# Kernel tuning notes

Hardware: AMD Instinct MI355X
Metric: run time of the kernel (lower is better)

Reference implementation:

```python
import jax, jax.numpy as jnp
import numpy as np

N, E, S, G = 524288, 2097152, 8192, 64
F_IN, HID = 64, 128


def setup_inputs() -> dict:
    key = jax.random.key(0)
    ks = jax.random.split(key, 12)
    x = jax.random.normal(ks[0], (N, F_IN), dtype=jnp.float32)
    edge_index = jax.random.randint(ks[1], (2, E), 0, N, dtype=jnp.int64)
    node_batch = jnp.sort(jax.random.randint(ks[2], (N,), 0, S, dtype=jnp.int64))
    weights = jax.random.uniform(ks[3], (S, 1), dtype=jnp.float32)
    subgraph_batch = jnp.sort(jax.random.randint(ks[4], (S,), 0, G, dtype=jnp.int64))
    s = 1.0 / np.sqrt(F_IN)
    h = 1.0 / np.sqrt(HID)
    W_l = jax.random.uniform(ks[5], (F_IN, HID), jnp.float32, -s, s)
    W_r = jax.random.uniform(ks[6], (F_IN, HID), jnp.float32, -s, s)
    b_conv = jax.random.uniform(ks[7], (HID,), jnp.float32, -s, s)
    W1 = jax.random.uniform(ks[8], (HID, HID), jnp.float32, -h, h)
    b1 = jax.random.uniform(ks[9], (HID,), jnp.float32, -h, h)
    W2 = jax.random.uniform(ks[10], (HID, 1), jnp.float32, -h, h)
    b2 = jax.random.uniform(ks[11], (1,), jnp.float32, -h, h)
    return {"x": x, "edge_index": edge_index, "node_batch": node_batch,
            "weights": weights, "subgraph_batch": subgraph_batch,
            "W_l": W_l, "W_r": W_r, "b_conv": b_conv,
            "W1": W1, "b1": b1, "W2": W2, "b2": b2}


def reference(x, edge_index, node_batch, weights, subgraph_batch,
              W_l, W_r, b_conv, W1, b1, W2, b2):
    src, dst = edge_index[0], edge_index[1]
    # GraphSAGE mean aggregation: gather neighbor feats, scatter-mean to dst
    msg_sum = jax.ops.segment_sum(x[src], dst, num_segments=N)  # [N, F_IN]
    deg = jax.ops.segment_sum(jnp.ones((E,), x.dtype), dst, num_segments=N)
    agg = msg_sum / jnp.maximum(deg, 1.0)[:, None]
    h = jax.nn.relu(agg @ W_l + x @ W_r + b_conv)               # [N, HID]
    # global_add_pool nodes -> subgraph embeddings
    g = jax.ops.segment_sum(h, node_batch, num_segments=S)      # [S, HID]
    # MLP head -> scalar per subgraph
    s = jax.nn.leaky_relu(g @ W1 + b1, negative_slope=0.01) @ W2 + b2  # [S, 1]
    sw = s * weights
    energy = jax.ops.segment_sum(sw, subgraph_batch, num_segments=G)   # [G, 1]
    norm = jax.ops.segment_sum(weights, subgraph_batch, num_segments=G)
    return energy / norm
```

## Files before the change

### kernel.cpp

```cpp
#include <hip/hip_runtime.h>
#include <hip/hip_bf16.h>

#define NN 524288
#define NE 2097152
#define NS 8192
#define NG 64
#define FIN 64
#define HIDDEN 128

#define NB 512
#define BIN_NODES 1024
#define CAP 4608

typedef __attribute__((ext_vector_type(8))) unsigned short ushort8;
typedef __attribute__((ext_vector_type(4))) unsigned short ushort4v;
typedef __attribute__((ext_vector_type(8))) short bf16x8;
typedef __attribute__((ext_vector_type(4))) float floatx4;

__device__ __forceinline__ unsigned short f2b(float f) {
  union { float f; unsigned int u; } c; c.f = f;
  unsigned int u = c.u;
  unsigned int r = (u + 0x7FFFu + ((u >> 16) & 1u)) >> 16;
  return (unsigned short)r;
}
__device__ __forceinline__ float b2f(unsigned short b) {
  union { unsigned int u; float f; } c; c.u = ((unsigned int)b) << 16;
  return c.f;
}

__global__ __launch_bounds__(256) void k_cast(const float* __restrict__ x,
                                              unsigned short* __restrict__ xb) {
  size_t i = ((size_t)blockIdx.x * 256 + threadIdx.x) * 8;
  float4 v0 = *(const float4*)(x + i);
  float4 v1 = *(const float4*)(x + i + 4);
  ushort8 r;
  r[0] = f2b(v0.x); r[1] = f2b(v0.y); r[2] = f2b(v0.z); r[3] = f2b(v0.w);
  r[4] = f2b(v1.x); r[5] = f2b(v1.y); r[6] = f2b(v1.z); r[7] = f2b(v1.w);
  *(ushort8*)(xb + i) = r;
}

__global__ __launch_bounds__(256) void k_prepw(const float* __restrict__ Wl,
                                               const float* __restrict__ Wr,
                                               unsigned short* __restrict__ Wt) {
  int i = blockIdx.x * 256 + threadIdx.x;
  int n = i >> 7, k = i & 127;
  float v = (k < FIN) ? Wl[k * HIDDEN + n] : Wr[(k - FIN) * HIDDEN + n];
  Wt[n * HIDDEN + k] = f2b(v);
}

__global__ __launch_bounds__(256) void k_bin1(const int* __restrict__ ei,
                                              int* __restrict__ binCursor,
                                              unsigned int* __restrict__ pairs) {
  __shared__ unsigned int pk[4096];
  __shared__ unsigned short bn[4096];
  __shared__ int cnt[NB];
  __shared__ int base[NB];
  const int t = threadIdx.x;
  const int eBase = blockIdx.x * 4096;
  cnt[t] = 0; cnt[t + 256] = 0;
  __syncthreads();
#pragma unroll
  for (int i = 0; i < 16; ++i) {
    int j = i * 256 + t;
    int e = eBase + j;
    int src = ei[e];
    int dst = ei[NE + e];
    int bin = dst >> 10;
    pk[j] = ((unsigned int)(dst & 1023) << 19) | (unsigned int)src;
    bn[j] = (unsigned short)bin;
    atomicAdd(&cnt[bin], 1);
  }
  __syncthreads();
  {
    int c0 = cnt[t], c1 = cnt[t + 256];
    base[t]       = atomicAdd(&binCursor[t], c0);
    base[t + 256] = atomicAdd(&binCursor[t + 256], c1);
    cnt[t] = 0; cnt[t + 256] = 0;
  }
  __syncthreads();
#pragma unroll
  for (int i = 0; i < 16; ++i) {
    int j = i * 256 + t;
    int bin = bn[j];
    int ofs = atomicAdd(&cnt[bin], 1);
    pairs[(size_t)bin * CAP + base[bin] + ofs] = pk[j];
  }
}

__global__ __launch_bounds__(256) void k_bin2(const int* __restrict__ binCursor,
                                              unsigned int* __restrict__ pairs,
                                              int* __restrict__ S) {
  __shared__ unsigned int pk[CAP];
  __shared__ int cnt[BIN_NODES];
  __shared__ int ps[256];
  const int t = threadIdx.x;
  const int b = blockIdx.x;
  int total = binCursor[b];
  if (total > CAP) total = CAP;
  const int gbase = b * CAP;

  for (int i = t; i < total; i += 256) pk[i] = pairs[gbase + i];
  cnt[t] = 0; cnt[t + 256] = 0; cnt[t + 512] = 0; cnt[t + 768] = 0;
  __syncthreads();

  for (int i = t; i < total; i += 256) atomicAdd(&cnt[pk[i] >> 19], 1);
  __syncthreads();

  int c0 = cnt[4 * t], c1 = cnt[4 * t + 1], c2 = cnt[4 * t + 2], c3 = cnt[4 * t + 3];
  int tot4 = c0 + c1 + c2 + c3;
  ps[t] = tot4;
  __syncthreads();
  for (int off = 1; off < 256; off <<= 1) {
    int v = 0;
    if (t >= off) v = ps[t - off];
    __syncthreads();
    ps[t] += v;
    __syncthreads();
  }
  int e0 = ps[t] - tot4;
  int e1 = e0 + c0, e2 = e1 + c1, e3 = e2 + c2;
  cnt[4 * t] = e0; cnt[4 * t + 1] = e1; cnt[4 * t + 2] = e2; cnt[4 * t + 3] = e3;
  int sidx = b * (BIN_NODES + 1) + 4 * t;
  S[sidx]     = gbase + e0;
  S[sidx + 1] = gbase + e1;
  S[sidx + 2] = gbase + e2;
  S[sidx + 3] = gbase + e3;
  if (t == 0) S[b * (BIN_NODES + 1) + BIN_NODES] = gbase + total;
  __syncthreads();

  for (int i = t; i < total; i += 256) {
    unsigned int p = pk[i];
    int dl = p >> 19;
    int ofs = atomicAdd(&cnt[dl], 1);
    pairs[gbase + ofs] = p & 0x7FFFFu;
  }
}

__global__ __launch_bounds__(256) void k_aggregate(const unsigned short* __restrict__ xb,
                                                   const int* __restrict__ S,
                                                   const unsigned int* __restrict__ bucket,
                                                   unsigned short* __restrict__ msgb) {
  const int t = threadIdx.x;
  const int grp = t >> 3;
  const int lane = t & 7;
  const int n = blockIdx.x * 32 + grp;
  const int sidx = n + (n >> 10);
  const int rp0 = S[sidx];
  const int rp1 = S[sidx + 1];

  float a0[8] = {0,0,0,0,0,0,0,0};
  float a1[8] = {0,0,0,0,0,0,0,0};
  float a2[8] = {0,0,0,0,0,0,0,0};
  float a3[8] = {0,0,0,0,0,0,0,0};
  int e = rp0;
  for (; e + 3 < rp1; e += 4) {
    int s0 = bucket[e], s1 = bucket[e + 1], s2 = bucket[e + 2], s3 = bucket[e + 3];
    ushort8 v0 = *(const ushort8*)(xb + (size_t)s0 * FIN + (lane << 3));
    ushort8 v1 = *(const ushort8*)(xb + (size_t)s1 * FIN + (lane << 3));
    ushort8 v2 = *(const ushort8*)(xb + (size_t)s2 * FIN + (lane << 3));
    ushort8 v3 = *(const ushort8*)(xb + (size_t)s3 * FIN + (lane << 3));
#pragma unroll
    for (int j = 0; j < 8; ++j) {
      a0[j] += b2f(v0[j]); a1[j] += b2f(v1[j]);
      a2[j] += b2f(v2[j]); a3[j] += b2f(v3[j]);
    }
  }
  for (; e < rp1; ++e) {
    int s0 = bucket[e];
    ushort8 v0 = *(const ushort8*)(xb + (size_t)s0 * FIN + (lane << 3));
#pragma unroll
    for (int j = 0; j < 8; ++j) a0[j] += b2f(v0[j]);
  }
  float rdeg = 1.f / fmaxf((float)(rp1 - rp0), 1.f);
  ushort8 r;
#pragma unroll
  for (int j = 0; j < 8; ++j)
    r[j] = f2b((a0[j] + a1[j] + a2[j] + a3[j]) * rdeg);
  *(ushort8*)(msgb + (size_t)n * FIN + (lane << 3)) = r;
}

#define CB_NODES 128
__global__ __launch_bounds__(256) void k_conv(const unsigned short* __restrict__ msgb,
                                              const unsigned short* __restrict__ xb,
                                              const int* __restrict__ node_batch,
                                              const unsigned short* __restrict__ Wt,
                                              const float* __restrict__ bconv,
                                              float* __restrict__ g) {
  __shared__ unsigned short As[128 * 136];
  __shared__ unsigned short Ws[128 * 136];
  __shared__ int nb_s[CB_NODES];
  const int t = threadIdx.x;
  const int n0 = blockIdx.x * CB_NODES;

  if (t < CB_NODES) nb_s[t] = node_batch[n0 + t];

#pragma unroll
  for (int it = 0; it < 8; ++it) {
    int i = it * 256 + t;
    int n = i >> 4;
    int c = i & 15;
    const unsigned short* src = (c < 8)
        ? msgb + (size_t)(n0 + n) * FIN + c * 8
        : xb + (size_t)(n0 + n) * FIN + (c - 8) * 8;
    *(ushort8*)(As + n * 136 + c * 8) = *(const ushort8*)src;
    *(ushort8*)(Ws + n * 136 + c * 8) = *(const ushort8*)(Wt + n * HIDDEN + c * 8);
  }
  __syncthreads();

  const int wave = t >> 6;
  const int lane = t & 63;
  const int l16 = lane & 15;
  const int quad = lane >> 4;

  floatx4 acc[2][8];
#pragma unroll
  for (int mt = 0; mt < 2; ++mt)
#pragma unroll
    for (int nt = 0; nt < 8; ++nt) acc[mt][nt] = (floatx4){0.f, 0.f, 0.f, 0.f};

  float bv[8];
#pragma unroll
  for (int nt = 0; nt < 8; ++nt) bv[nt] = bconv[nt * 16 + l16];

#pragma unroll
  for (int ks = 0; ks < 4; ++ks) {
    bf16x8 a0 = *(const bf16x8*)(As + (wave * 32 + l16) * 136 + ks * 32 + quad * 8);
    bf16x8 a1 = *(const bf16x8*)(As + (wave * 32 + 16 + l16) * 136 + ks * 32 + quad * 8);
#pragma unroll
    for (int nt = 0; nt < 8; ++nt) {
      bf16x8 b = *(const bf16x8*)(Ws + (nt * 16 + l16) * 136 + ks * 32 + quad * 8);
      acc[0][nt] = __builtin_amdgcn_mfma_f32_16x16x32_bf16(a0, b, acc[0][nt], 0, 0, 0);
      acc[1][nt] = __builtin_amdgcn_mfma_f32_16x16x32_bf16(a1, b, acc[1][nt], 0, 0, 0);
    }
  }

#pragma unroll
  for (int mt = 0; mt < 2; ++mt)
#pragma unroll
    for (int nt = 0; nt < 8; ++nt) {
      int col = nt * 16 + l16;
#pragma unroll
      for (int r = 0; r < 4; ++r) {
        int row = wave * 32 + mt * 16 + quad * 4 + r;
        float hv = fmaxf(acc[mt][nt][r] + bv[nt], 0.f);
        As[row * 136 + col] = f2b(hv);
      }
    }
  __syncthreads();

  {
    int j = t & 127;
    int half = t >> 7;
    int ns = half * 64, ne = ns + 64;
    float sum = 0.f;
    int cur = nb_s[ns];
    for (int n = ns; n < ne; ++n) {
      int b = nb_s[n];
      if (b != cur) {
        unsafeAtomicAdd(&g[(size_t)cur * HIDDEN + j], sum);
        sum = 0.f;
        cur = b;
      }
      sum += b2f(As[n * 136 + j]);
    }
    unsafeAtomicAdd(&g[(size_t)cur * HIDDEN + j], sum);
  }
}

__global__ __launch_bounds__(256) void k_head(const float* __restrict__ g,
                                              const float* __restrict__ W1,
                                              const float* __restrict__ b1,
                                              const float* __restrict__ W2,
                                              const float* __restrict__ b2,
                                              const float* __restrict__ wts,
                                              const int* __restrict__ sgb,
                                              float* __restrict__ egy,
                                              float* __restrict__ nrm) {
  int s = blockIdx.x * 4 + (threadIdx.x >> 6);
  int lane = threadIdx.x & 63;
  const float* grow = g + (size_t)s * HIDDEN;
  float acc0 = b1[lane];
  float acc1 = b1[lane + 64];
  for (int k = 0; k < HIDDEN; ++k) {
    float gk = grow[k];
    acc0 = fmaf(gk, W1[k * HIDDEN + lane], acc0);
    acc1 = fmaf(gk, W1[k * HIDDEN + 64 + lane], acc1);
  }
  float t0 = acc0 > 0.f ? acc0 : 0.01f * acc0;
  float t1 = acc1 > 0.f ? acc1 : 0.01f * acc1;
  float part = t0 * W2[lane] + t1 * W2[lane + 64];
#pragma unroll
  for (int off = 32; off > 0; off >>= 1) part += __shfl_down(part, off, 64);
  if (lane == 0) {
    float sval = part + b2[0];
    float w = wts[s];
    int grp = sgb[s];
    unsafeAtomicAdd(&egy[grp], sval * w);
    unsafeAtomicAdd(&nrm[grp], w);
  }
}

__global__ void k_final(const float* __restrict__ egy,
                        const float* __restrict__ nrm,
                        float* __restrict__ out) {
  int t = threadIdx.x;
  out[t] = egy[t] / nrm[t];
}

extern "C" void kernel_launch(void* const* d_in, const int* in_sizes, int n_in,
                              void* d_out, int out_size, void* d_ws, size_t ws_size,
                              hipStream_t stream) {
  const float* x   = (const float*)d_in[0];
  const int*   ei  = (const int*)d_in[1];
  const int*   nb  = (const int*)d_in[2];
  const float* wts = (const float*)d_in[3];
  const int*   sgb = (const int*)d_in[4];
  const float* Wl  = (const float*)d_in[5];
  const float* Wr  = (const float*)d_in[6];
  const float* bcv = (const float*)d_in[7];
  const float* W1  = (const float*)d_in[8];
  const float* b1  = (const float*)d_in[9];
  const float* W2  = (const float*)d_in[10];
  const float* b2  = (const float*)d_in[11];
  float* out = (float*)d_out;

  int*   binCursor = (int*)d_ws;
  float* g         = (float*)(binCursor + NB);
  float* egy       = g + (size_t)NS * HIDDEN;
  float* nrm       = egy + NG;
  int*   S         = (int*)(nrm + NG);
  unsigned int* pairs = (unsigned int*)(S + NB * (BIN_NODES + 1));
  unsigned short* xb   = (unsigned short*)(pairs + (size_t)NB * CAP);
  unsigned short* msgb = xb + (size_t)NN * FIN;
  unsigned short* Wt   = msgb + (size_t)NN * FIN;

  size_t zero_bytes = ((size_t)NB + (size_t)NS * HIDDEN + 2 * NG) * 4;
  hipMemsetAsync(d_ws, 0, zero_bytes, stream);

  k_cast <<<(NN * FIN) / (256 * 8), 256, 0, stream>>>(x, xb);
  k_prepw<<<64, 256, 0, stream>>>(Wl, Wr, Wt);
  k_bin1 <<<NE / 4096, 256, 0, stream>>>(ei, binCursor, pairs);
  k_bin2 <<<NB, 256, 0, stream>>>(binCursor, pairs, S);
  k_aggregate<<<NN / 32, 256, 0, stream>>>(xb, S, pairs, msgb);
  k_conv<<<NN / CB_NODES, 256, 0, stream>>>(msgb, xb, nb, Wt, bcv, g);
  k_head<<<NS / 4, 256, 0, stream>>>(g, W1, b1, W2, b2, wts, sgb, egy, nrm);
  k_final<<<1, 64, 0, stream>>>(egy, nrm, out);
}
```

Measured before the change: 479.9 us.

## Hold weight fragments in registers and widen conv blocks to 512 threads

The conv kernel no longer stages the 128x128 weight tile in shared memory. Each of eight waves now loads its own 16-column slice of the weights straight into registers and loops over all eight 16-row tiles, with the block size going from 256 to 512 threads. This roughly halves shared memory per block and removes the weight copy and its LDS reads, which should allow more resident blocks. The cost is more global weight loads per block (mostly L2 hits) and a segmented pool reduction split into four 32-node quarters, which can issue more atomics.

```diff
diff --git a/kernel.cpp b/kernel.cpp
--- a/kernel.cpp
+++ b/kernel.cpp
@@ -180,14 +180,13 @@
 }
 
 #define CB_NODES 128
-__global__ __launch_bounds__(256) void k_conv(const unsigned short* __restrict__ msgb,
-                                              const unsigned short* __restrict__ xb,
-                                              const int* __restrict__ node_batch,
-                                              const unsigned short* __restrict__ Wt,
-                                              const float* __restrict__ bconv,
-                                              float* __restrict__ g) {
+__global__ __launch_bounds__(512, 6) void k_conv(const unsigned short* __restrict__ msgb,
+                                                 const unsigned short* __restrict__ xb,
+                                                 const int* __restrict__ node_batch,
+                                                 const unsigned short* __restrict__ Wt,
+                                                 const float* __restrict__ bconv,
+                                                 float* __restrict__ g) {
   __shared__ unsigned short As[128 * 136];
-  __shared__ unsigned short Ws[128 * 136];
   __shared__ int nb_s[CB_NODES];
   const int t = threadIdx.x;
   const int n0 = blockIdx.x * CB_NODES;
@@ -195,63 +194,61 @@
   if (t < CB_NODES) nb_s[t] = node_batch[n0 + t];
 
 #pragma unroll
-  for (int it = 0; it < 8; ++it) {
-    int i = it * 256 + t;
+  for (int it = 0; it < 4; ++it) {
+    int i = it * 512 + t;
     int n = i >> 4;
     int c = i & 15;
     const unsigned short* src = (c < 8)
         ? msgb + (size_t)(n0 + n) * FIN + c * 8
         : xb + (size_t)(n0 + n) * FIN + (c - 8) * 8;
     *(ushort8*)(As + n * 136 + c * 8) = *(const ushort8*)src;
-    *(ushort8*)(Ws + n * 136 + c * 8) = *(const ushort8*)(Wt + n * HIDDEN + c * 8);
-  }
-  __syncthreads();
+  }
 
   const int wave = t >> 6;
   const int lane = t & 63;
   const int l16 = lane & 15;
   const int quad = lane >> 4;
 
-  floatx4 acc[2][8];
-#pragma unroll
-  for (int mt = 0; mt < 2; ++mt)
-#pragma unroll
-    for (int nt = 0; nt < 8; ++nt) acc[mt][nt] = (floatx4){0.f, 0.f, 0.f, 0.f};
-
-  float bv[8];
-#pragma unroll
-  for (int nt = 0; nt < 8; ++nt) bv[nt] = bconv[nt * 16 + l16];
-
-#pragma unroll
-  for (int ks = 0; ks < 4; ++ks) {
-    bf16x8 a0 = *(const bf16x8*)(As + (wave * 32 + l16) * 136 + ks * 32 + quad * 8);
-    bf16x8 a1 = *(const bf16x8*)(As + (wave * 32 + 16 + l16) * 136 + ks * 32 + quad * 8);
-#pragma unroll
-    for (int nt = 0; nt < 8; ++nt) {
-      bf16x8 b = *(const bf16x8*)(Ws + (nt * 16 + l16) * 136 + ks * 32 + quad * 8);
-      acc[0][nt] = __builtin_amdgcn_mfma_f32_16x16x32_bf16(a0, b, acc[0][nt], 0, 0, 0);
-      acc[1][nt] = __builtin_amdgcn_mfma_f32_16x16x32_bf16(a1, b, acc[1][nt], 0, 0, 0);
+  bf16x8 bfrag[4];
+#pragma unroll
+  for (int ks = 0; ks < 4; ++ks)
+    bfrag[ks] = *(const bf16x8*)(Wt + (size_t)(wave * 16 + l16) * HIDDEN + ks * 32 + quad * 8);
+  float bv = bconv[wave * 16 + l16];
+
+  floatx4 acc[8];
+#pragma unroll
+  for (int mt = 0; mt < 8; ++mt) acc[mt] = (floatx4){0.f, 0.f, 0.f, 0.f};
+
+  __syncthreads();
+
+#pragma unroll
+  for (int mt = 0; mt < 8; ++mt) {
+#pragma unroll
+    for (int ks = 0; ks < 4; ++ks) {
+      bf16x8 a = *(const bf16x8*)(As + (mt * 16 + l16) * 136 + ks * 32 + quad * 8);
+      acc[mt] = __builtin_amdgcn_mfma_f32_16x16x32_bf16(a, bfrag[ks], acc[mt], 0, 0, 0);
     }
   }
 
-#pragma unroll
-  for (int mt = 0; mt < 2; ++mt)
-#pragma unroll
-    for (int nt = 0; nt < 8; ++nt) {
-      int col = nt * 16 + l16;
+  __syncthreads();
+
+  {
+    int col = wave * 16 + l16;
+#pragma unroll
+    for (int mt = 0; mt < 8; ++mt)
 #pragma unroll
       for (int r = 0; r < 4; ++r) {
-        int row = wave * 32 + mt * 16 + quad * 4 + r;
-        float hv = fmaxf(acc[mt][nt][r] + bv[nt], 0.f);
+        int row = mt * 16 + quad * 4 + r;
+        float hv = fmaxf(acc[mt][r] + bv, 0.f);
         As[row * 136 + col] = f2b(hv);
       }
-    }
+  }
   __syncthreads();
 
   {
     int j = t & 127;
-    int half = t >> 7;
-    int ns = half * 64, ne = ns + 64;
+    int q = t >> 7;
+    int ns = q * 32, ne = ns + 32;
     float sum = 0.f;
     int cur = nb_s[ns];
     for (int n = ns; n < ne; ++n) {
@@ -342,7 +339,7 @@
   k_bin1 <<<NE / 4096, 256, 0, stream>>>(ei, binCursor, pairs);
   k_bin2 <<<NB, 256, 0, stream>>>(binCursor, pairs, S);
   k_aggregate<<<NN / 32, 256, 0, stream>>>(xb, S, pairs, msgb);
-  k_conv<<<NN / CB_NODES, 256, 0, stream>>>(msgb, xb, nb, Wt, bcv, g);
+  k_conv<<<NN / CB_NODES, 512, 0, stream>>>(msgb, xb, nb, Wt, bcv, g);
   k_head<<<NS / 4, 256, 0, stream>>>(g, W1, b1, W2, b2, wts, sgb, egy, nrm);
   k_final<<<1, 64, 0, stream>>>(egy, nrm, out);
 }
```

Result: faster. 441.3 us (-8.0%).
